# Optimization experiments

Measured on AMD Instinct MI355X. Metric: run time of the kernel, lower is better.

## Reference

```python
import jax, jax.numpy as jnp
import numpy as np

RANK = 100
NUM_ITEMS = 6714
BATCH = 8192


def setup_inputs() -> dict:
    key = jax.random.key(0)
    k1, k2 = jax.random.split(key)
    output = jax.random.normal(k1, (BATCH, NUM_ITEMS), dtype=jnp.float32)
    labels = jax.random.randint(k2, (BATCH,), 0, NUM_ITEMS)
    return {"output": output, "labels": labels}


def reference(output, labels):
    # output: [B, N] float logits; labels: [B] int
    rank = RANK
    # torch: output.argsort(1)[:, -rank:] -> top-rank indices in ASCENDING value order.
    # Efficient form: top_k (descending) then flip along the rank axis.
    _, top_idx = jax.lax.top_k(output, rank)          # [B, rank] descending
    target_indices = top_idx[:, ::-1]                 # ascending, matches argsort slice

    label_where = target_indices == labels[:, None]   # [B, rank]
    has_label = label_where.any(axis=1)               # [B]

    # For rows where the label is not in the top-rank set, overwrite slot 0 with the label.
    col0 = jnp.arange(rank)[None, :] == 0             # [1, rank]
    target_indices = jnp.where((~has_label)[:, None] & col0,
                               labels[:, None], target_indices)

    new_output = jnp.take_along_axis(output, target_indices, axis=1)  # [B, rank]

    # Position of label in target_indices (label occurs at most once per row);
    # argmax of the boolean mask gives that position, and 0 when absent -- which
    # matches torch (zeros_like, only rows with the label get overwritten).
    new_labels = jnp.argmax(label_where, axis=1)      # [B]
    return new_output, new_labels
```

## Files before the change

### kernel.cpp

```cpp
#include <hip/hip_runtime.h>


#define NROWS 8192
#define NCOLS 6714
#define NC2   3357
#define K     100
#define CAP   512
#define BLK   256

__device__ __forceinline__ unsigned int flip32(float v) {
    unsigned int b = __float_as_uint(v);
    return ((int)b < 0) ? ~b : (b | 0x80000000u);
}
__device__ __forceinline__ float unflip32(unsigned int k) {
    unsigned int b = (k & 0x80000000u) ? (k ^ 0x80000000u) : ~k;
    return __uint_as_float(b);
}

__global__ __launch_bounds__(BLK) void logit_selector_kernel(
    const float* __restrict__ out_mat,
    const int*   __restrict__ labels,
    float*       __restrict__ new_out,
    float*       __restrict__ new_lab)
{
    __shared__ unsigned long long ckey[CAP];
    __shared__ unsigned int s_cnum;
    __shared__ int          s_lab;
    __shared__ int          s_has;

    const int row  = blockIdx.x;
    const int tid  = threadIdx.x;
    const int lane = tid & 63;
    const float*  __restrict__ rp  = out_mat + (size_t)row * NCOLS;
    const float2* __restrict__ rp2 = (const float2*)rp;

    if (tid == 0) { s_has = 0; s_lab = 0; }

    float lo = -50.0f, hi = 50.0f;
    float t  = 1.9f;
    unsigned int cnt;
    for (int attempt = 0; ; ++attempt) {
        if (tid == 0) s_cnum = 0;
        __syncthreads();

        #pragma unroll 4
        for (int i = tid; i < NC2; i += BLK) {
            float2 v2 = rp2[i];
            if (v2.x > t) {
                unsigned int p = atomicAdd(&s_cnum, 1u);
                if (p < CAP)
                    ckey[p] = ((unsigned long long)flip32(v2.x) << 32)
                            | (unsigned int)~(unsigned int)(2 * i);
            }
            if (v2.y > t) {
                unsigned int p = atomicAdd(&s_cnum, 1u);
                if (p < CAP)
                    ckey[p] = ((unsigned long long)flip32(v2.y) << 32)
                            | (unsigned int)~(unsigned int)(2 * i + 1);
            }
        }
        __syncthreads();
        cnt = s_cnum;
        if ((cnt >= K && cnt <= CAP) || attempt >= 62) break;
        if (cnt < (unsigned int)K) hi = t; else lo = t;
        t = 0.5f * (lo + hi);
        __syncthreads();
    }

    const int C    = (int)min(cnt, (unsigned int)CAP);
    const int Cpad = (C + 63) & ~63;

    for (int c = C + tid; c < Cpad; c += BLK) ckey[c] = 0ULL;
    __syncthreads();

    const int label = labels[row];

    for (int jbase = 0; jbase < C; jbase += BLK) {
        const int  j      = jbase + tid;
        const bool active = (j < C);
        const unsigned long long kj = active ? ckey[j] : 0ULL;
        int rank = 0;
        for (int cb = 0; cb < Cpad; cb += 64) {
            const unsigned long long kt = ckey[cb + lane];
            const unsigned int tlo = (unsigned int)kt;
            const unsigned int thi = (unsigned int)(kt >> 32);
            #pragma unroll
            for (int l = 0; l < 64; ++l) {
                const unsigned int clo = __builtin_amdgcn_readlane(tlo, l);
                const unsigned int chi = __builtin_amdgcn_readlane(thi, l);
                const unsigned long long kc =
                    ((unsigned long long)chi << 32) | clo;
                rank += (kc > kj);
            }
        }
        if (active && rank < K) {
            const int col = (K - 1) - rank;
            const float        vj = unflip32((unsigned int)(kj >> 32));
            const unsigned int ij = ~(unsigned int)kj;
            new_out[(size_t)row * K + col] = vj;
            if ((int)ij == label) { s_has = 1; s_lab = col; }
        }
    }
    __syncthreads();

    if (tid == 0) {
        int lab = s_lab;
        if (!s_has) {
            new_out[(size_t)row * K] = rp[label];
            lab = 0;
        }
        new_lab[row] = (float)lab;
    }
}

extern "C" void kernel_launch(void* const* d_in, const int* in_sizes, int n_in,
                              void* d_out, int out_size, void* d_ws, size_t ws_size,
                              hipStream_t stream) {
    const float* out_mat = (const float*)d_in[0];
    const int*   labels  = (const int*)d_in[1];
    float* new_out = (float*)d_out;
    float* new_lab = (float*)d_out + (size_t)NROWS * K;

    logit_selector_kernel<<<dim3(NROWS), dim3(BLK), 0, stream>>>(
        out_mat, labels, new_out, new_lab);
}
```

Baseline: 349.9 us.

## Cache row in registers, use 32-bit rank keys with duplicate fallback

Each thread now loads its slice of the row into registers once, so repeated threshold passes no longer re-read global memory. The rank-counting loop compares 32-bit value keys instead of 64-bit value+index keys. An exact tie-break pass with the index runs only when duplicate values are detected. The bisection's second guess is also tuned to typical counts. In exchange, register pressure rises and the rare duplicate case costs an extra pass.

```diff
diff --git a/kernel.cpp b/kernel.cpp
--- a/kernel.cpp
+++ b/kernel.cpp
@@ -7,14 +7,14 @@
 #define K     100
 #define CAP   512
 #define BLK   256
+#define VPT   14
 
 __device__ __forceinline__ unsigned int flip32(float v) {
     unsigned int b = __float_as_uint(v);
     return ((int)b < 0) ? ~b : (b | 0x80000000u);
 }
 __device__ __forceinline__ float unflip32(unsigned int k) {
-    unsigned int b = (k & 0x80000000u) ? (k ^ 0x80000000u) : ~k;
-    return __uint_as_float(b);
+    return __uint_as_float((k & 0x80000000u) ? (k ^ 0x80000000u) : ~k);
 }
 
 __global__ __launch_bounds__(BLK) void logit_selector_kernel(
@@ -23,54 +23,52 @@
     float*       __restrict__ new_out,
     float*       __restrict__ new_lab)
 {
-    __shared__ unsigned long long ckey[CAP];
+    __shared__ unsigned int cvkey[CAP];
+    __shared__ unsigned int cidx[CAP];
     __shared__ unsigned int s_cnum;
-    __shared__ int          s_lab;
-    __shared__ int          s_has;
+    __shared__ int s_lab, s_has, s_dup;
 
     const int row  = blockIdx.x;
     const int tid  = threadIdx.x;
     const int lane = tid & 63;
-    const float*  __restrict__ rp  = out_mat + (size_t)row * NCOLS;
-    const float2* __restrict__ rp2 = (const float2*)rp;
+    const float2* __restrict__ rp2 = (const float2*)(out_mat + (size_t)row * NCOLS);
 
-    if (tid == 0) { s_has = 0; s_lab = 0; }
+    float2 v[VPT];
+    #pragma unroll
+    for (int k = 0; k < VPT - 1; ++k) v[k] = rp2[tid + k * BLK];
+    const bool hasLast = (tid + (VPT - 1) * BLK) < NC2;
+    v[VPT - 1] = hasLast ? rp2[tid + (VPT - 1) * BLK] : make_float2(-1e30f, -1e30f);
 
-    float lo = -50.0f, hi = 50.0f;
-    float t  = 1.9f;
+    if (tid == 0) { s_has = 0; s_lab = 0; s_dup = 0; }
+
+    float lo = -400.0f, hi = 400.0f, t = 2.1f;
     unsigned int cnt;
     for (int attempt = 0; ; ++attempt) {
         if (tid == 0) s_cnum = 0;
         __syncthreads();
-
-        #pragma unroll 4
-        for (int i = tid; i < NC2; i += BLK) {
-            float2 v2 = rp2[i];
-            if (v2.x > t) {
+        #pragma unroll
+        for (int k = 0; k < VPT; ++k) {
+            if (v[k].x > t) {
                 unsigned int p = atomicAdd(&s_cnum, 1u);
-                if (p < CAP)
-                    ckey[p] = ((unsigned long long)flip32(v2.x) << 32)
-                            | (unsigned int)~(unsigned int)(2 * i);
+                if (p < CAP) { cvkey[p] = flip32(v[k].x); cidx[p] = 2*(tid + k*BLK); }
             }
-            if (v2.y > t) {
+            if (v[k].y > t) {
                 unsigned int p = atomicAdd(&s_cnum, 1u);
-                if (p < CAP)
-                    ckey[p] = ((unsigned long long)flip32(v2.y) << 32)
-                            | (unsigned int)~(unsigned int)(2 * i + 1);
+                if (p < CAP) { cvkey[p] = flip32(v[k].y); cidx[p] = 2*(tid + k*BLK) + 1; }
             }
         }
         __syncthreads();
         cnt = s_cnum;
         if ((cnt >= K && cnt <= CAP) || attempt >= 62) break;
         if (cnt < (unsigned int)K) hi = t; else lo = t;
-        t = 0.5f * (lo + hi);
+        t = (attempt == 0) ? ((cnt < (unsigned int)K) ? 1.85f : 2.35f)
+                           : 0.5f * (lo + hi);
         __syncthreads();
     }
 
     const int C    = (int)min(cnt, (unsigned int)CAP);
     const int Cpad = (C + 63) & ~63;
-
-    for (int c = C + tid; c < Cpad; c += BLK) ckey[c] = 0ULL;
+    for (int c = C + tid; c < Cpad; c += BLK) { cvkey[c] = 0u; cidx[c] = 0xFFFFFFFFu; }
     __syncthreads();
 
     const int label = labels[row];
@@ -78,34 +76,63 @@
     for (int jbase = 0; jbase < C; jbase += BLK) {
         const int  j      = jbase + tid;
         const bool active = (j < C);
-        const unsigned long long kj = active ? ckey[j] : 0ULL;
-        int rank = 0;
+        if (__ballot(active) == 0) continue;
+        unsigned int kj = 0;
+        if (active) kj = cvkey[j];
+        int rank = 0, eqc = 0;
         for (int cb = 0; cb < Cpad; cb += 64) {
-            const unsigned long long kt = ckey[cb + lane];
-            const unsigned int tlo = (unsigned int)kt;
-            const unsigned int thi = (unsigned int)(kt >> 32);
+            const unsigned int kt = cvkey[cb + lane];
             #pragma unroll
             for (int l = 0; l < 64; ++l) {
-                const unsigned int clo = __builtin_amdgcn_readlane(tlo, l);
-                const unsigned int chi = __builtin_amdgcn_readlane(thi, l);
-                const unsigned long long kc =
-                    ((unsigned long long)chi << 32) | clo;
+                const unsigned int kc = __builtin_amdgcn_readlane(kt, l);
                 rank += (kc > kj);
+                eqc  += (kc == kj);
             }
         }
-        if (active && rank < K) {
-            const int col = (K - 1) - rank;
-            const float        vj = unflip32((unsigned int)(kj >> 32));
-            const unsigned int ij = ~(unsigned int)kj;
-            new_out[(size_t)row * K + col] = vj;
-            if ((int)ij == label) { s_has = 1; s_lab = col; }
+        if (active) {
+            if (eqc >= 2) s_dup = 1;
+            if (rank < K) {
+                const int col = (K - 1) - rank;
+                new_out[(size_t)row * K + col] = unflip32(kj);
+                if ((int)cidx[j] == label) { s_has = 1; s_lab = col; }
+            }
         }
     }
     __syncthreads();
 
+    if (s_dup) {
+        if (tid == 0) { s_has = 0; s_lab = 0; }
+        __syncthreads();
+        for (int jbase = 0; jbase < C; jbase += BLK) {
+            const int  j      = jbase + tid;
+            const bool active = (j < C);
+            if (__ballot(active) == 0) continue;
+            unsigned int kj = 0, ijx = 0xFFFFFFFFu;
+            if (active) { kj = cvkey[j]; ijx = cidx[j]; }
+            int rank = 0;
+            for (int cb = 0; cb < Cpad; cb += 64) {
+                const unsigned int kt = cvkey[cb + lane];
+                const unsigned int it = cidx[cb + lane];
+                #pragma unroll
+                for (int l = 0; l < 64; ++l) {
+                    const unsigned int kc = __builtin_amdgcn_readlane(kt, l);
+                    const unsigned int ic = __builtin_amdgcn_readlane(it, l);
+                    rank += (kc > kj) || (kc == kj && ic < ijx);
+                }
+            }
+            if (active && rank < K) {
+                const int col = (K - 1) - rank;
+                new_out[(size_t)row * K + col] = unflip32(kj);
+                if ((int)cidx[j] == label) { s_has = 1; s_lab = col; }
+            }
+        }
+        __syncthreads();
+    }
+
     if (tid == 0) {
         int lab = s_lab;
         if (!s_has) {
+            const float* rp = out_mat + (size_t)row * NCOLS;
             new_out[(size_t)row * K] = rp[label];
             lab = 0;
         }
```

After: 306.0 us. 12.6% less time.
